# Performance work log

Measured on AMD Instinct MI355X. Metric: run time of the kernel, lower is better.

The kernel has to match this reference:

```python
import jax, jax.numpy as jnp
import numpy as np

N_HEADS = 4
HEAD_DIM = 128
FMAP_H, FMAP_W = 32, 32
IN_DIM = 512
BATCH = 16


def setup_inputs() -> dict:
    key = jax.random.key(0)
    k1, k2, k3, k4 = jax.random.split(key, 4)
    scale = HEAD_DIM ** (-0.5)
    x = jax.random.normal(k1, (BATCH, IN_DIM, FMAP_H, FMAP_W), dtype=jnp.float32)
    # 1x1 conv weight producing q,k,v stacked along output channels
    conv_w = jax.random.normal(k2, (3 * N_HEADS * HEAD_DIM, IN_DIM), dtype=jnp.float32) * (IN_DIM ** -0.5)
    pos_h = jax.random.normal(k3, (FMAP_H, HEAD_DIM), dtype=jnp.float32) * scale
    pos_w = jax.random.normal(k4, (FMAP_W, HEAD_DIM), dtype=jnp.float32) * scale
    return {"x": x, "conv_w": conv_w, "pos_h": pos_h, "pos_w": pos_w}


def reference(x, conv_w, pos_h, pos_w):
    B, C, H, W = x.shape
    hw = H * W
    scale = HEAD_DIM ** (-0.5)
    # 1x1 conv == pointwise linear over channels
    qkv = jnp.einsum('bchw,oc->bohw', x, conv_w)               # [B, 3*nh*hd, H, W]
    qkv = qkv.reshape(B, 3, N_HEADS, HEAD_DIM, hw)             # chunk + per-head split
    q = jnp.swapaxes(qkv[:, 0], -1, -2) * scale                # [B, nh, hw, hd]
    k = jnp.swapaxes(qkv[:, 1], -1, -2)
    v = jnp.swapaxes(qkv[:, 2], -1, -2)
    # absolute positional embedding: h[i,:]+w[j,:] flattened over positions
    emb = (pos_h[:, None, :] + pos_w[None, :, :]).reshape(hw, HEAD_DIM)
    sim = jnp.einsum('bhid,bhjd->bhij', q, k) + jnp.einsum('bhid,jd->bhij', q, emb)
    attn = jax.nn.softmax(sim, axis=-1)
    out = jnp.einsum('bhij,bhjd->bhid', attn, v)               # [B, nh, hw, hd]
    out = jnp.swapaxes(out, -1, -2)                            # [B, nh, hd, hw]
    return out.reshape(B, N_HEADS * HEAD_DIM, hw // N_HEADS, N_HEADS)
```

## Files before the change

kernel.cpp:

```cpp
#include <hip/hip_runtime.h>

#define NB 16
#define NH 4
#define HD 128
#define HW 1024
#define CIN 512

typedef short s16x8 __attribute__((ext_vector_type(8)));
typedef short s16x4 __attribute__((ext_vector_type(4)));
typedef float f32x4 __attribute__((ext_vector_type(4)));

static __device__ __forceinline__ short f2bf(float f) {
    union { float f; unsigned u; } v; v.f = f;
    unsigned r = v.u + 0x7fffu + ((v.u >> 16) & 1u);
    return (short)(r >> 16);
}

static __device__ __forceinline__ void gload16(const short* g, short* l) {
    __builtin_amdgcn_global_load_lds(
        (const __attribute__((address_space(1))) unsigned int*)g,
        (__attribute__((address_space(3))) unsigned int*)l, 16, 0, 0);
}

__global__ __launch_bounds__(256) void prep_xw(
    const float* __restrict__ x, const float* __restrict__ w,
    short* __restrict__ xT, short* __restrict__ Wb)
{
    int blk = blockIdx.x;
    if (blk < NB * 16 * 32) {
        int b = blk >> 9, rem = blk & 511;
        int ct = rem >> 5, pt = rem & 31;
        __shared__ float tile[32][33];
        int tc = threadIdx.x >> 5;
        int tp = threadIdx.x & 31;
        const float* xb = x + ((size_t)b * CIN + ct * 32) * HW + pt * 32;
        #pragma unroll
        for (int i = 0; i < 4; i++)
            tile[tc + i * 8][tp] = xb[(size_t)(tc + i * 8) * HW + tp];
        __syncthreads();
        int p = threadIdx.x >> 3, cq = threadIdx.x & 7;
        short* xo = xT + ((size_t)b * HW + pt * 32 + p) * CIN + ct * 32 + cq * 4;
        s16x4 o4 = { f2bf(tile[cq * 4 + 0][p]), f2bf(tile[cq * 4 + 1][p]),
                     f2bf(tile[cq * 4 + 2][p]), f2bf(tile[cq * 4 + 3][p]) };
        *reinterpret_cast<s16x4*>(xo) = o4;
    } else {
        int wb = blk - NB * 16 * 32;
        size_t base = (size_t)wb * 1024 + threadIdx.x * 4;
        const float4 v = *reinterpret_cast<const float4*>(w + base);
        s16x4 o4 = { f2bf(v.x), f2bf(v.y), f2bf(v.z), f2bf(v.w) };
        *reinterpret_cast<s16x4*>(Wb + base) = o4;
    }
}

__global__ __launch_bounds__(256, 3) void qkv_proj(
    const short* __restrict__ xT, const short* __restrict__ Wb,
    const float* __restrict__ pos_h, const float* __restrict__ pos_w,
    short* __restrict__ Q, short* __restrict__ Kp, short* __restrict__ Vt)
{
    __shared__ __align__(1024) char smem[34816];
    short* As = (short*)smem;
    short* Bs = As + 128 * 64;
    short* vb = (short*)smem;

    const int pt = blockIdx.x, ot = blockIdx.y, b = blockIdx.z;
    const int tid = threadIdx.x;
    const int wave = tid >> 6, lane = tid & 63;
    const int l16 = lane & 15, quad = lane >> 4;
    const int wm = (wave & 1) * 64, wn = (wave >> 1) * 64;
    const int o0 = ot * 128, p0 = pt * 128;

    const short* xb = xT + (size_t)b * HW * CIN;

    const int r8 = lane >> 3, c8 = lane & 7;
    const int sch = c8 ^ r8;
    const short* wsrc = Wb + (size_t)(o0 + wave * 32 + r8) * CIN + sch * 8;
    const short* xsrc = xb + (size_t)(p0 + wave * 32 + r8) * CIN + sch * 8;
    short* adst = As + wave * 2048;
    short* bdst = Bs + wave * 2048;

    f32x4 acc[4][4];
    #pragma unroll
    for (int i = 0; i < 4; i++)
        #pragma unroll
        for (int j = 0; j < 4; j++)
            acc[i][j] = f32x4{0.f, 0.f, 0.f, 0.f};

    #pragma unroll 1
    for (int kc = 0; kc < CIN; kc += 64) {
        #pragma unroll
        for (int j = 0; j < 4; j++) {
            gload16(wsrc + kc + (size_t)(j * 8) * CIN, adst + j * 512);
            gload16(xsrc + kc + (size_t)(j * 8) * CIN, bdst + j * 512);
        }
        __syncthreads();
        #pragma unroll
        for (int kk = 0; kk < 2; kk++) {
            s16x8 aF[4], bF[4];
            #pragma unroll
            for (int mi = 0; mi < 4; mi++)
                aF[mi] = *(const s16x8*)(As + (wm + mi * 16 + l16) * 64
                                         + (((kk * 4 + quad) ^ (l16 & 7)) * 8));
            #pragma unroll
            for (int ni = 0; ni < 4; ni++)
                bF[ni] = *(const s16x8*)(Bs + (wn + ni * 16 + l16) * 64
                                         + (((kk * 4 + quad) ^ (l16 & 7)) * 8));
            #pragma unroll
            for (int mi = 0; mi < 4; mi++)
                #pragma unroll
                for (int ni = 0; ni < 4; ni++)
                    acc[mi][ni] = __builtin_amdgcn_mfma_f32_16x16x32_bf16(
                        aF[mi], bF[ni], acc[mi][ni], 0, 0, 0);
        }
        __syncthreads();
    }

    const int s = ot >> 2, h = ot & 3;
    const size_t bh = (size_t)(b * NH + h);

    if (s == 0) {
        const float qs = 0.08838834764831845f * 1.4426950408889634f;
        short* Qb = Q + bh * (size_t)(HW * HD);
        #pragma unroll
        for (int mi = 0; mi < 4; mi++) {
            int d0 = wm + mi * 16 + quad * 4;
            #pragma unroll
            for (int ni = 0; ni < 4; ni++) {
                int p = p0 + wn + ni * 16 + l16;
                f32x4 a = acc[mi][ni];
                s16x4 o4 = { f2bf(a.x * qs), f2bf(a.y * qs),
                             f2bf(a.z * qs), f2bf(a.w * qs) };
                *reinterpret_cast<s16x4*>(Qb + (size_t)p * HD + d0) = o4;
            }
        }
    } else if (s == 1) {
        short* Kb = Kp + bh * (size_t)(HW * HD);
        #pragma unroll
        for (int mi = 0; mi < 4; mi++) {
            int d0 = wm + mi * 16 + quad * 4;
            #pragma unroll
            for (int ni = 0; ni < 4; ni++) {
                int p = p0 + wn + ni * 16 + l16;
                const float4 eh = *reinterpret_cast<const float4*>(pos_h + (p >> 5) * HD + d0);
                const float4 ew = *reinterpret_cast<const float4*>(pos_w + (p & 31) * HD + d0);
                f32x4 a = acc[mi][ni];
                s16x4 o4 = { f2bf(a.x + eh.x + ew.x), f2bf(a.y + eh.y + ew.y),
                             f2bf(a.z + eh.z + ew.z), f2bf(a.w + eh.w + ew.w) };
                *reinterpret_cast<s16x4*>(Kb + (size_t)p * HD + d0) = o4;
            }
        }
    } else {
        __syncthreads();
        #pragma unroll
        for (int mi = 0; mi < 4; mi++) {
            int d0 = wm + mi * 16 + quad * 4;
            #pragma unroll
            for (int ni = 0; ni < 4; ni++) {
                int p = wn + ni * 16 + l16;
                f32x4 a = acc[mi][ni];
                vb[(d0 + 0) * 136 + p] = f2bf(a.x);
                vb[(d0 + 1) * 136 + p] = f2bf(a.y);
                vb[(d0 + 2) * 136 + p] = f2bf(a.z);
                vb[(d0 + 3) * 136 + p] = f2bf(a.w);
            }
        }
        __syncthreads();
        short* Vb = Vt + bh * (size_t)(HD * HW);
        int d = tid >> 1, half = tid & 1;
        #pragma unroll
        for (int j = 0; j < 8; j++) {
            const short* row = vb + d * 136;
            int base = (half * 2 + (j >> 2)) * 32 + (j & 3) * 4;
            s16x4 lo = *(const s16x4*)(row + base);
            s16x4 hi = *(const s16x4*)(row + base + 16);
            s16x8 v8 = { lo[0], lo[1], lo[2], lo[3],
                         hi[0], hi[1], hi[2], hi[3] };
            *reinterpret_cast<s16x8*>(Vb + (size_t)d * HW + p0 + half * 64 + j * 8) = v8;
        }
    }
}

__global__ __launch_bounds__(256, 2) void attn_fused(
    const short* __restrict__ Q, const short* __restrict__ Kp,
    const short* __restrict__ Vt, float* __restrict__ out)
{
    __shared__ __align__(16) short Ks[2][64 * 128];
    __shared__ __align__(16) short Vs[2][128 * 64];

    const int flat = blockIdx.x;
    const int qt = flat >> 6;
    const int bh = flat & 63;
    const int tid = threadIdx.x;
    const int wave = tid >> 6, lane = tid & 63;
    const int l16 = lane & 15, quad = lane >> 4;

    const short* Qb = Q + (size_t)bh * (HW * HD);
    const short* Kb = Kp + (size_t)bh * (HW * HD);
    const short* Vb = Vt + (size_t)bh * (HD * HW);

    const int q0 = qt * 128 + wave * 32;

    s16x8 bQ[2][4];
    #pragma unroll
    for (int nt = 0; nt < 2; nt++)
        #pragma unroll
        for (int kk = 0; kk < 4; kk++)
            bQ[nt][kk] = *(const s16x8*)(Qb + (size_t)(q0 + nt * 16 + l16) * HD
                                         + kk * 32 + quad * 8);

    s16x8 ones;
    #pragma unroll
    for (int j = 0; j < 8; j++) ones[j] = (short)0x3F80;

    f32x4 Oacc[2][8];
    #pragma unroll
    for (int mt = 0; mt < 2; mt++)
        #pragma unroll
        for (int dt = 0; dt < 8; dt++)
            Oacc[mt][dt] = f32x4{0.f, 0.f, 0.f, 0.f};
    f32x4 lacc[2] = { f32x4{0.f, 0.f, 0.f, 0.f}, f32x4{0.f, 0.f, 0.f, 0.f} };

    const int kKey = tid >> 4, kC = tid & 15;
    const int kPhys = kC ^ kKey;
    const short* kgp = Kb + (size_t)kKey * HD + kC * 8;
    const int kOff = kKey * 128 + kPhys * 8;
    const int vD = tid >> 3, vC = tid & 7;
    const int vPhys = vC ^ (vD & 7);
    const short* vgp = Vb + (size_t)vD * HW + vC * 8;
    const int vOff = vD * 64 + vPhys * 8;

    s16x8 kreg[4], vreg[4];
    #pragma unroll
    for (int i = 0; i < 4; i++) {
        kreg[i] = *(const s16x8*)(kgp + (size_t)(i * 16) * HD);
        vreg[i] = *(const s16x8*)(vgp + (size_t)(i * 32) * HW);
    }
    #pragma unroll
    for (int i = 0; i < 4; i++) {
        *(s16x8*)(&Ks[0][kOff] + i * 16 * 128) = kreg[i];
        *(s16x8*)(&Vs[0][vOff] + i * 32 * 64) = vreg[i];
    }
    #pragma unroll
    for (int i = 0; i < 4; i++) {
        kreg[i] = *(const s16x8*)(kgp + (size_t)(64 + i * 16) * HD);
        vreg[i] = *(const s16x8*)(vgp + 64 + (size_t)(i * 32) * HW);
    }
    __syncthreads();

    #pragma unroll 1
    for (int kt = 0; kt < 16; kt++) {
        const int cur = kt & 1, nxt = cur ^ 1;
        const short* ks = Ks[cur];
        const short* vs = Vs[cur];

        #pragma unroll
        for (int i = 0; i < 4; i++) {
            *(s16x8*)(&Ks[nxt][kOff] + i * 16 * 128) = kreg[i];
            *(s16x8*)(&Vs[nxt][vOff] + i * 32 * 64) = vreg[i];
        }
        int ktn = (kt + 2) & 15;
        #pragma unroll
        for (int i = 0; i < 4; i++) {
            kreg[i] = *(const s16x8*)(kgp + (size_t)(ktn * 64 + i * 16) * HD);
            vreg[i] = *(const s16x8*)(vgp + ktn * 64 + (size_t)(i * 32) * HW);
        }

        f32x4 c[4][2];
        __builtin_amdgcn_s_setprio(1);
        #pragma unroll
        for (int mtp = 0; mtp < 4; mtp++) {
            s16x8 aK[4];
            #pragma unroll
            for (int kk = 0; kk < 4; kk++)
                aK[kk] = *(const s16x8*)(ks + (mtp * 16 + l16) * 128
                                         + (((kk * 4 + quad) ^ l16) * 8));
            c[mtp][0] = f32x4{0.f, 0.f, 0.f, 0.f};
            c[mtp][1] = f32x4{0.f, 0.f, 0.f, 0.f};
            #pragma unroll
            for (int kk = 0; kk < 4; kk++) {
                c[mtp][0] = __builtin_amdgcn_mfma_f32_16x16x32_bf16(
                    aK[kk], bQ[0][kk], c[mtp][0], 0, 0, 0);
                c[mtp][1] = __builtin_amdgcn_mfma_f32_16x16x32_bf16(
                    aK[kk], bQ[1][kk], c[mtp][1], 0, 0, 0);
            }
        }
        __builtin_amdgcn_s_setprio(0);

        #pragma unroll
        for (int h = 0; h < 2; h++) {
            s16x8 aP[2];
            #pragma unroll
            for (int mt = 0; mt < 2; mt++) {
                f32x4 e0 = c[2 * h][mt], e1 = c[2 * h + 1][mt];
                aP[mt] = s16x8{
                    f2bf(__builtin_amdgcn_exp2f(e0[0])),
                    f2bf(__builtin_amdgcn_exp2f(e0[1])),
                    f2bf(__builtin_amdgcn_exp2f(e0[2])),
                    f2bf(__builtin_amdgcn_exp2f(e0[3])),
                    f2bf(__builtin_amdgcn_exp2f(e1[0])),
                    f2bf(__builtin_amdgcn_exp2f(e1[1])),
                    f2bf(__builtin_amdgcn_exp2f(e1[2])),
                    f2bf(__builtin_amdgcn_exp2f(e1[3])) };
            }

            __builtin_amdgcn_s_setprio(1);
            #pragma unroll
            for (int mt = 0; mt < 2; mt++)
                lacc[mt] = __builtin_amdgcn_mfma_f32_16x16x32_bf16(
                    aP[mt], ones, lacc[mt], 0, 0, 0);

            #pragma unroll
            for (int dt = 0; dt < 8; dt++) {
                s16x8 bV = *(const s16x8*)(vs + (dt * 16 + l16) * 64
                                           + (((h * 4 + quad) ^ (l16 & 7)) * 8));
                #pragma unroll
                for (int mt = 0; mt < 2; mt++)
                    Oacc[mt][dt] = __builtin_amdgcn_mfma_f32_16x16x32_bf16(
                        aP[mt], bV, Oacc[mt][dt], 0, 0, 0);
            }
            __builtin_amdgcn_s_setprio(0);
        }
        __syncthreads();
    }

    float* ob = out + (size_t)bh * (HD * HW);
    #pragma unroll
    for (int mt = 0; mt < 2; mt++) {
        float inv[4];
        #pragma unroll
        for (int r = 0; r < 4; r++) inv[r] = __builtin_amdgcn_rcpf(lacc[mt][r]);
        int prow = q0 + mt * 16 + quad * 4;
        #pragma unroll
        for (int dt = 0; dt < 8; dt++) {
            int d = dt * 16 + l16;
            f32x4 o = Oacc[mt][dt];
            float4 o4 = { o[0] * inv[0], o[1] * inv[1],
                          o[2] * inv[2], o[3] * inv[3] };
            *reinterpret_cast<float4*>(ob + (size_t)d * HW + prow) = o4;
        }
    }
}

extern "C" void kernel_launch(void* const* d_in, const int* in_sizes, int n_in,
                              void* d_out, int out_size, void* d_ws, size_t ws_size,
                              hipStream_t stream) {
    const float* x  = (const float*)d_in[0];
    const float* w  = (const float*)d_in[1];
    const float* ph = (const float*)d_in[2];
    const float* pw = (const float*)d_in[3];

    const size_t BHPD = (size_t)NB * NH * HW * HD;
    short* Q    = (short*)d_ws;
    short* Kp   = Q + BHPD;
    short* Vt   = Kp + BHPD;
    short* xT   = Vt + BHPD;
    short* Wb   = xT + (size_t)NB * HW * CIN;
    float* outp = (float*)d_out;

    prep_xw<<<dim3(NB * 16 * 32 + 768), 256, 0, stream>>>(x, w, xT, Wb);
    qkv_proj<<<dim3(8, 12, NB), 256, 0, stream>>>(xT, Wb, ph, pw, Q, Kp, Vt);
    attn_fused<<<dim3(512), 256, 0, stream>>>(Q, Kp, Vt, outp);
}
```

Before: 164.2 us.

## Load K/V tiles directly into LDS with global_load_lds instead of registers

Replaces the register-staged K/V double buffering (global load to VGPRs, then ds_write one tile later) with direct global-to-LDS async loads, keeping the XOR swizzle by permuting the global source addresses. Prefetch distance drops from two tiles (one in registers, one in LDS) to one tile ahead in LDS. The aim is to free VGPRs and remove the ds_write instructions from the loop. The risk is that less latency is hidden, and the waits for the async loads before __syncthreads are only implicit.

```diff
diff --git a/kernel.cpp b/kernel.cpp
--- a/kernel.cpp
+++ b/kernel.cpp
@@ -183,8 +183,8 @@
     const short* __restrict__ Q, const short* __restrict__ Kp,
     const short* __restrict__ Vt, float* __restrict__ out)
 {
-    __shared__ __align__(16) short Ks[2][64 * 128];
-    __shared__ __align__(16) short Vs[2][128 * 64];
+    __shared__ __align__(1024) short Ks[2][64 * 128];
+    __shared__ __align__(1024) short Vs[2][128 * 64];
 
     const int flat = blockIdx.x;
     const int qt = flat >> 6;
@@ -219,31 +219,25 @@
             Oacc[mt][dt] = f32x4{0.f, 0.f, 0.f, 0.f};
     f32x4 lacc[2] = { f32x4{0.f, 0.f, 0.f, 0.f}, f32x4{0.f, 0.f, 0.f, 0.f} };
 
-    const int kKey = tid >> 4, kC = tid & 15;
-    const int kPhys = kC ^ kKey;
-    const short* kgp = Kb + (size_t)kKey * HD + kC * 8;
-    const int kOff = kKey * 128 + kPhys * 8;
-    const int vD = tid >> 3, vC = tid & 7;
-    const int vPhys = vC ^ (vD & 7);
-    const short* vgp = Vb + (size_t)vD * HW + vC * 8;
-    const int vOff = vD * 64 + vPhys * 8;
-
-    s16x8 kreg[4], vreg[4];
-    #pragma unroll
-    for (int i = 0; i < 4; i++) {
-        kreg[i] = *(const s16x8*)(kgp + (size_t)(i * 16) * HD);
-        vreg[i] = *(const s16x8*)(vgp + (size_t)(i * 32) * HW);
-    }
-    #pragma unroll
-    for (int i = 0; i < 4; i++) {
-        *(s16x8*)(&Ks[0][kOff] + i * 16 * 128) = kreg[i];
-        *(s16x8*)(&Vs[0][vOff] + i * 32 * 64) = vreg[i];
-    }
-    #pragma unroll
-    for (int i = 0; i < 4; i++) {
-        kreg[i] = *(const s16x8*)(kgp + (size_t)(64 + i * 16) * HD);
-        vreg[i] = *(const s16x8*)(vgp + 64 + (size_t)(i * 32) * HW);
-    }
+    const int kRow = lane >> 4;
+    const int vRow = lane >> 3;
+    const int vSch = (lane & 7) ^ vRow;
+
+    #define STAGE(buf, tile)                                                  \
+        do {                                                                  \
+            _Pragma("unroll")                                                 \
+            for (int j = 0; j < 4; j++) {                                     \
+                int kkey = wave * 16 + j * 4 + kRow;                          \
+                gload16(Kb + ((size_t)((tile) * 64 + kkey)) * HD              \
+                           + (((lane & 15) ^ (j * 4 + kRow)) * 8),            \
+                        &Ks[buf][(wave * 16 + j * 4) * 128] + lane * 8);      \
+                int vd = wave * 32 + j * 8 + vRow;                            \
+                gload16(Vb + (size_t)vd * HW + (tile) * 64 + vSch * 8,        \
+                        &Vs[buf][(wave * 32 + j * 8) * 64] + lane * 8);       \
+            }                                                                 \
+        } while (0)
+
+    STAGE(0, 0);
     __syncthreads();
 
     #pragma unroll 1
@@ -252,17 +246,7 @@
         const short* ks = Ks[cur];
         const short* vs = Vs[cur];
 
-        #pragma unroll
-        for (int i = 0; i < 4; i++) {
-            *(s16x8*)(&Ks[nxt][kOff] + i * 16 * 128) = kreg[i];
-            *(s16x8*)(&Vs[nxt][vOff] + i * 32 * 64) = vreg[i];
-        }
-        int ktn = (kt + 2) & 15;
-        #pragma unroll
-        for (int i = 0; i < 4; i++) {
-            kreg[i] = *(const s16x8*)(kgp + (size_t)(ktn * 64 + i * 16) * HD);
-            vreg[i] = *(const s16x8*)(vgp + ktn * 64 + (size_t)(i * 32) * HW);
-        }
+        STAGE(nxt, (kt + 1) & 15);
 
         f32x4 c[4][2];
         __builtin_amdgcn_s_setprio(1);
@@ -321,6 +305,7 @@
         }
         __syncthreads();
     }
+    #undef STAGE
 
     float* ob = out + (size_t)bh * (HD * HW);
     #pragma unroll
```

After: 167.7 us. +2.1%, slower.
